# Kernel optimization log

Measured on AMD Instinct MI355X. Metric: run time of the kernel, lower is better.

## Reference

```python
import jax, jax.numpy as jnp
import numpy as np

DIM = 384
HEADS = 12
WS = 7            # per-side window size (sqrt of 49)
TOK = WS * WS     # tokens per window = 49


def _relative_position_index():
    coords = np.stack(np.meshgrid(np.arange(WS), np.arange(WS), indexing='ij'))  # [2,ws,ws]
    flat = coords.reshape(2, -1)                                                  # [2,49]
    rel = flat[:, :, None] - flat[:, None, :]                                     # [2,49,49]
    rel = rel.transpose(1, 2, 0)
    rel[:, :, 0] += WS - 1
    rel[:, :, 1] += WS - 1
    rel[:, :, 0] *= 2 * WS - 1
    return rel.sum(-1).astype(np.int32)                                           # [49,49]


def setup_inputs() -> dict:
    key = jax.random.key(0)
    ks = jax.random.split(key, 6)
    B, N, C = 32, 3136, DIM
    x = jax.random.normal(ks[0], (B, N, C), dtype=jnp.float32)
    qkv_w = jax.random.normal(ks[1], (C, 3 * C), dtype=jnp.float32) * 0.02
    qkv_b = jnp.zeros((3 * C,), dtype=jnp.float32)
    proj_w = jax.random.normal(ks[2], (C, C), dtype=jnp.float32) * 0.02
    proj_b = jnp.zeros((C,), dtype=jnp.float32)
    n_bias = (2 * WS - 1) * (2 * WS - 1)  # 169
    rel_bias_table = jax.random.normal(ks[3], (n_bias, HEADS), dtype=jnp.float32) * 0.02
    rel_index = jnp.asarray(_relative_position_index())
    return {"x": x, "qkv_w": qkv_w, "qkv_b": qkv_b, "proj_w": proj_w,
            "proj_b": proj_b, "rel_bias_table": rel_bias_table, "rel_index": rel_index}


def reference(x, qkv_w, qkv_b, proj_w, proj_b, rel_bias_table, rel_index):
    B, N, C = x.shape
    H, d = HEADS, C // HEADS
    L = N // TOK                      # number of windows per batch element
    scale = d ** (-0.5)

    qkv = x @ qkv_w + qkv_b                              # [B,N,3C]
    qkv = qkv.reshape(B * L, TOK, 3, H, d)               # non-shuffle layout: (L ws1 ws2)
    q = jnp.transpose(qkv[:, :, 0], (0, 2, 1, 3)) * scale  # [BL,H,49,d]
    k = jnp.transpose(qkv[:, :, 1], (0, 2, 1, 3))
    v = jnp.transpose(qkv[:, :, 2], (0, 2, 1, 3))

    attn = jnp.einsum('whqd,whkd->whqk', q, k)           # [BL,H,49,49]
    bias = rel_bias_table[rel_index.reshape(-1)].reshape(TOK, TOK, H)
    bias = jnp.transpose(bias, (2, 0, 1))                # [H,49,49]
    attn = jax.nn.softmax(attn + bias[None], axis=-1)

    out = jnp.einsum('whqk,whkd->whqd', attn, v)         # [BL,H,49,d]
    out = jnp.transpose(out, (0, 2, 1, 3)).reshape(B, N, C)
    return out @ proj_w + proj_b
```

## Files before the change

### kernel.cpp

```cpp
#include <hip/hip_runtime.h>
#include <stdint.h>

#define TOK 49
#define NTOK 100352
#define K3 1152
#define C_DIM 384
#define NHEAD 12

typedef _Float16 half8 __attribute__((ext_vector_type(8)));
typedef float f32x4 __attribute__((ext_vector_type(4)));

__device__ __forceinline__ ushort f2h_bits(float f) {
  _Float16 h = (_Float16)f;
  return __builtin_bit_cast(ushort, h);
}

__device__ __forceinline__ void gload_lds16(const void* gp, void* lp) {
  __builtin_amdgcn_global_load_lds(
      (const __attribute__((address_space(1))) void*)gp,
      (__attribute__((address_space(3))) void*)lp, 16, 0, 0);
}

__global__ __launch_bounds__(256) void cvt_f32_f16(const float* __restrict__ in,
                                                   _Float16* __restrict__ out, int n4) {
  int i = blockIdx.x * 256 + threadIdx.x;
  if (i >= n4) return;
  float4 v = *((const float4*)in + i);
  ushort4 o;
  o.x = f2h_bits(v.x); o.y = f2h_bits(v.y); o.z = f2h_bits(v.z); o.w = f2h_bits(v.w);
  *((ushort4*)out + i) = o;
}

__global__ __launch_bounds__(256) void transpose_to_f16(const float* __restrict__ in,
                                                        _Float16* __restrict__ out,
                                                        int R, int Cc) {
  int idx = blockIdx.x * 256 + threadIdx.x;
  if (idx >= R * Cc) return;
  int n = idx / R, k = idx - n * R;
  out[idx] = (_Float16)in[(size_t)k * Cc + n];
}

__global__ __launch_bounds__(256) void bias_expand(const float* __restrict__ table,
                                                   const int* __restrict__ relidx,
                                                   float* __restrict__ out) {
  int idx = blockIdx.x * 256 + threadIdx.x;
  if (idx >= NHEAD * TOK * TOK) return;
  int h = idx / (TOK * TOK);
  int qk = idx - h * (TOK * TOK);
  out[idx] = table[relidx[qk] * NHEAD + h];
}

template <int OUT_F32>
__global__ __launch_bounds__(256) void gemm_f16(const _Float16* __restrict__ A,
                                                const _Float16* __restrict__ Bt,
                                                const float* __restrict__ bias,
                                                void* __restrict__ Cout,
                                                int N, int K, int Ntiles) {
  __shared__ _Float16 As[128 * 32];
  __shared__ _Float16 Bs[128 * 32];
  int bid = blockIdx.x;
  int bm = bid / Ntiles, bn = bid - bm * Ntiles;
  int tid = threadIdx.x;
  int lane = tid & 63, wave = tid >> 6;
  int wm = wave >> 1, wn = wave & 1;

  int srow = tid >> 2;
  int scol = (tid & 3) * 8;
  const _Float16* gA = A + (size_t)(bm * 128 + srow) * K + scol;
  const _Float16* gB = Bt + (size_t)(bn * 128 + srow) * K + scol;
  char* ldsA = (char*)As + wave * 1024;
  char* ldsB = (char*)Bs + wave * 1024;

  f32x4 acc[4][4];
#pragma unroll
  for (int m = 0; m < 4; m++)
#pragma unroll
    for (int n = 0; n < 4; n++) acc[m][n] = (f32x4){0.f, 0.f, 0.f, 0.f};

  int fr = lane & 15;
  int fk = (lane >> 4) * 8;

  for (int k0 = 0; k0 < K; k0 += 32) {
    __syncthreads();
    gload_lds16(gA + k0, ldsA);
    gload_lds16(gA + (size_t)64 * K + k0, ldsA + 4096);
    gload_lds16(gB + k0, ldsB);
    gload_lds16(gB + (size_t)64 * K + k0, ldsB + 4096);
    __syncthreads();
    half8 af[4], bf[4];
#pragma unroll
    for (int m = 0; m < 4; m++)
      af[m] = *(const half8*)(As + (wm * 64 + m * 16 + fr) * 32 + fk);
#pragma unroll
    for (int n = 0; n < 4; n++)
      bf[n] = *(const half8*)(Bs + (wn * 64 + n * 16 + fr) * 32 + fk);
#pragma unroll
    for (int m = 0; m < 4; m++)
#pragma unroll
      for (int n = 0; n < 4; n++)
        acc[m][n] = __builtin_amdgcn_mfma_f32_16x16x32_f16(af[m], bf[n], acc[m][n], 0, 0, 0);
  }

  int rowbase = bm * 128 + wm * 64;
  int colbase = bn * 128 + wn * 64;
#pragma unroll
  for (int n = 0; n < 4; n++) {
    int col = colbase + n * 16 + fr;
    float bb = bias[col];
#pragma unroll
    for (int m = 0; m < 4; m++) {
      int row0 = rowbase + m * 16 + (lane >> 4) * 4;
#pragma unroll
      for (int r = 0; r < 4; r++) {
        float v = acc[m][n][r] + bb;
        if (OUT_F32)
          ((float*)Cout)[(size_t)(row0 + r) * N + col] = v;
        else
          ((ushort*)Cout)[(size_t)(row0 + r) * N + col] = f2h_bits(v);
      }
    }
  }
}

__global__ __launch_bounds__(256) void win_attn(const _Float16* __restrict__ qkv,
                                                const float* __restrict__ biasf,
                                                _Float16* __restrict__ aout) {
  __shared__ _Float16 P[4][64 * 72];
  int lane = threadIdx.x & 63, wave = threadIdx.x >> 6;
  int id = blockIdx.x * 4 + wave;
  int win = id / NHEAD;
  int h = id - win * NHEAD;
  const _Float16* base = qkv + (size_t)win * TOK * K3 + h * 32;
  int fr = lane & 15, fg = lane >> 4;

  half8 qf[4], kf[4];
#pragma unroll
  for (int i = 0; i < 4; i++) {
    int q = i * 16 + fr;
    qf[i] = (half8){0, 0, 0, 0, 0, 0, 0, 0};
    kf[i] = (half8){0, 0, 0, 0, 0, 0, 0, 0};
    if (q < TOK) {
      qf[i] = *(const half8*)(base + (size_t)q * K3 + fg * 8);
      kf[i] = *(const half8*)(base + (size_t)q * K3 + 384 + fg * 8);
    }
  }

  f32x4 s[4][4];
#pragma unroll
  for (int i = 0; i < 4; i++)
#pragma unroll
    for (int j = 0; j < 4; j++) s[i][j] = (f32x4){0.f, 0.f, 0.f, 0.f};
#pragma unroll
  for (int i = 0; i < 4; i++)
#pragma unroll
    for (int j = 0; j < 4; j++)
      s[i][j] = __builtin_amdgcn_mfma_f32_16x16x32_f16(qf[i], kf[j], s[i][j], 0, 0, 0);

  const float scale = 0.17677669529663687f;
  const float* bh = biasf + h * (TOK * TOK);
#pragma unroll
  for (int i = 0; i < 4; i++) {
#pragma unroll
    for (int r = 0; r < 4; r++) {
      int q = i * 16 + fg * 4 + r;
      float vals[4];
      float rowm = -1e30f;
#pragma unroll
      for (int j = 0; j < 4; j++) {
        int kk = j * 16 + fr;
        float v = -1e30f;
        if (q < TOK && kk < TOK) v = s[i][j][r] * scale + bh[q * TOK + kk];
        vals[j] = v;
        rowm = fmaxf(rowm, v);
      }
#pragma unroll
      for (int md = 1; md < 16; md <<= 1) rowm = fmaxf(rowm, __shfl_xor(rowm, md, 64));
      float rs = 0.f;
#pragma unroll
      for (int j = 0; j < 4; j++) { vals[j] = __expf(vals[j] - rowm); rs += vals[j]; }
#pragma unroll
      for (int md = 1; md < 16; md <<= 1) rs += __shfl_xor(rs, md, 64);
      float iv = 1.0f / rs;
#pragma unroll
      for (int j = 0; j < 4; j++)
        P[wave][q * 72 + j * 16 + fr] = (_Float16)(vals[j] * iv);
    }
  }

  half8 vf[2][2];
#pragma unroll
  for (int n = 0; n < 2; n++)
#pragma unroll
    for (int kx = 0; kx < 2; kx++) {
#pragma unroll
      for (int e = 0; e < 8; e++) {
        int kk = kx * 32 + fg * 8 + e;
        _Float16 vv = (_Float16)0.f;
        if (kk < TOK) vv = base[(size_t)kk * K3 + 768 + n * 16 + fr];
        vf[n][kx][e] = vv;
      }
    }

  f32x4 o[4][2];
#pragma unroll
  for (int i = 0; i < 4; i++)
#pragma unroll
    for (int n = 0; n < 2; n++) o[i][n] = (f32x4){0.f, 0.f, 0.f, 0.f};
#pragma unroll
  for (int i = 0; i < 4; i++) {
    half8 pf0 = *(const half8*)(&P[wave][(i * 16 + fr) * 72 + fg * 8]);
    half8 pf1 = *(const half8*)(&P[wave][(i * 16 + fr) * 72 + 32 + fg * 8]);
#pragma unroll
    for (int n = 0; n < 2; n++) {
      o[i][n] = __builtin_amdgcn_mfma_f32_16x16x32_f16(pf0, vf[n][0], o[i][n], 0, 0, 0);
      o[i][n] = __builtin_amdgcn_mfma_f32_16x16x32_f16(pf1, vf[n][1], o[i][n], 0, 0, 0);
    }
  }

  _Float16* obase = aout + (size_t)win * TOK * C_DIM + h * 32;
#pragma unroll
  for (int i = 0; i < 4; i++)
#pragma unroll
    for (int n = 0; n < 2; n++)
#pragma unroll
      for (int r = 0; r < 4; r++) {
        int q = i * 16 + fg * 4 + r;
        if (q < TOK) obase[(size_t)q * C_DIM + n * 16 + fr] = (_Float16)o[i][n][r];
      }
}

extern "C" void kernel_launch(void* const* d_in, const int* in_sizes, int n_in,
                              void* d_out, int out_size, void* d_ws, size_t ws_size,
                              hipStream_t stream) {
  const float* x = (const float*)d_in[0];
  const float* qkv_w = (const float*)d_in[1];
  const float* qkv_b = (const float*)d_in[2];
  const float* proj_w = (const float*)d_in[3];
  const float* proj_b = (const float*)d_in[4];
  const float* rel_table = (const float*)d_in[5];
  const int* rel_index = (const int*)d_in[6];

  char* ws = (char*)d_ws;
  _Float16* ws_x    = (_Float16*)(ws + 0);
  _Float16* ws_qkv  = (_Float16*)(ws + 77070336);
  _Float16* ws_attn = (_Float16*)(ws + 308281344);
  _Float16* ws_wT   = (_Float16*)(ws + 385351680);
  _Float16* ws_pT   = (_Float16*)(ws + 386236416);
  float*    ws_bias = (float*)(ws + 386531328);

  cvt_f32_f16<<<37632, 256, 0, stream>>>(x, ws_x, 9633792);
  transpose_to_f16<<<1728, 256, 0, stream>>>(qkv_w, ws_wT, 384, 1152);
  transpose_to_f16<<<576, 256, 0, stream>>>(proj_w, ws_pT, 384, 384);
  bias_expand<<<113, 256, 0, stream>>>(rel_table, rel_index, ws_bias);

  gemm_f16<0><<<7056, 256, 0, stream>>>(ws_x, ws_wT, qkv_b, ws_qkv, 1152, 384, 9);
  win_attn<<<6144, 256, 0, stream>>>(ws_qkv, ws_bias, ws_attn);
  gemm_f16<1><<<2352, 256, 0, stream>>>(ws_attn, ws_pT, proj_b, (void*)d_out, 384, 384, 3);
}
```

Baseline: 607.7 us.

## Double-buffer GEMM LDS tiles and hoist V loads in window attention

The GEMM kernel now keeps two LDS buffers for the A and B tiles and issues the global-to-LDS loads for the next K step before computing on the current one. This replaces the two barriers per iteration with a single waitcnt+barrier, aiming to overlap memory latency with MFMA work. The attention kernel also issues its scattered V gathers at the start, so their latency overlaps the QK^T and softmax phase. The cost is doubled LDS per GEMM block, which may lower occupancy, and more live registers in the attention kernel.

New measurement: 605.0 us. Within noise of the previous version (-0.4%).

```diff
diff --git a/kernel.cpp b/kernel.cpp
--- a/kernel.cpp
+++ b/kernel.cpp
@@ -56,8 +56,8 @@
                                                 const float* __restrict__ bias,
                                                 void* __restrict__ Cout,
                                                 int N, int K, int Ntiles) {
-  __shared__ _Float16 As[128 * 32];
-  __shared__ _Float16 Bs[128 * 32];
+  __shared__ _Float16 As[2][128 * 32];
+  __shared__ _Float16 Bs[2][128 * 32];
   int bid = blockIdx.x;
   int bm = bid / Ntiles, bn = bid - bm * Ntiles;
   int tid = threadIdx.x;
@@ -68,8 +68,6 @@
   int scol = (tid & 3) * 8;
   const _Float16* gA = A + (size_t)(bm * 128 + srow) * K + scol;
   const _Float16* gB = Bt + (size_t)(bn * 128 + srow) * K + scol;
-  char* ldsA = (char*)As + wave * 1024;
-  char* ldsB = (char*)Bs + wave * 1024;
 
   f32x4 acc[4][4];
 #pragma unroll
@@ -79,26 +77,40 @@
 
   int fr = lane & 15;
   int fk = (lane >> 4) * 8;
-
-  for (int k0 = 0; k0 < K; k0 += 32) {
-    __syncthreads();
-    gload_lds16(gA + k0, ldsA);
-    gload_lds16(gA + (size_t)64 * K + k0, ldsA + 4096);
-    gload_lds16(gB + k0, ldsB);
-    gload_lds16(gB + (size_t)64 * K + k0, ldsB + 4096);
-    __syncthreads();
+  int nk = K >> 5;
+
+  auto STAGE = [&](int buf, int k0) {
+    char* la = (char*)As[buf] + wave * 1024;
+    char* lb = (char*)Bs[buf] + wave * 1024;
+    gload_lds16(gA + k0, la);
+    gload_lds16(gA + (size_t)64 * K + k0, la + 4096);
+    gload_lds16(gB + k0, lb);
+    gload_lds16(gB + (size_t)64 * K + k0, lb + 4096);
+  };
+
+  STAGE(0, 0);
+  asm volatile("s_waitcnt vmcnt(0)" ::: "memory");
+  __builtin_amdgcn_s_barrier();
+
+  for (int t = 0; t < nk; t++) {
+    int cur = t & 1;
+    if (t + 1 < nk) STAGE(cur ^ 1, (t + 1) * 32);
     half8 af[4], bf[4];
 #pragma unroll
     for (int m = 0; m < 4; m++)
-      af[m] = *(const half8*)(As + (wm * 64 + m * 16 + fr) * 32 + fk);
+      af[m] = *(const half8*)(As[cur] + (wm * 64 + m * 16 + fr) * 32 + fk);
 #pragma unroll
     for (int n = 0; n < 4; n++)
-      bf[n] = *(const half8*)(Bs + (wn * 64 + n * 16 + fr) * 32 + fk);
+      bf[n] = *(const half8*)(Bs[cur] + (wn * 64 + n * 16 + fr) * 32 + fk);
 #pragma unroll
     for (int m = 0; m < 4; m++)
 #pragma unroll
       for (int n = 0; n < 4; n++)
         acc[m][n] = __builtin_amdgcn_mfma_f32_16x16x32_f16(af[m], bf[n], acc[m][n], 0, 0, 0);
+    if (t + 1 < nk) {
+      asm volatile("s_waitcnt vmcnt(0)" ::: "memory");
+      __builtin_amdgcn_s_barrier();
+    }
   }
 
   int rowbase = bm * 128 + wm * 64;
@@ -133,6 +145,20 @@
   const _Float16* base = qkv + (size_t)win * TOK * K3 + h * 32;
   int fr = lane & 15, fg = lane >> 4;
 
+  half8 vf[2][2];
+#pragma unroll
+  for (int n = 0; n < 2; n++)
+#pragma unroll
+    for (int kx = 0; kx < 2; kx++) {
+#pragma unroll
+      for (int e = 0; e < 8; e++) {
+        int kk = kx * 32 + fg * 8 + e;
+        _Float16 vv = (_Float16)0.f;
+        if (kk < TOK) vv = base[(size_t)kk * K3 + 768 + n * 16 + fr];
+        vf[n][kx][e] = vv;
+      }
+    }
+
   half8 qf[4], kf[4];
 #pragma unroll
   for (int i = 0; i < 4; i++) {
@@ -186,20 +212,6 @@
         P[wave][q * 72 + j * 16 + fr] = (_Float16)(vals[j] * iv);
     }
   }
-
-  half8 vf[2][2];
-#pragma unroll
-  for (int n = 0; n < 2; n++)
-#pragma unroll
-    for (int kx = 0; kx < 2; kx++) {
-#pragma unroll
-      for (int e = 0; e < 8; e++) {
-        int kk = kx * 32 + fg * 8 + e;
-        _Float16 vv = (_Float16)0.f;
-        if (kk < TOK) vv = base[(size_t)kk * K3 + 768 + n * 16 + fr];
-        vf[n][kx][e] = vv;
-      }
-    }
 
   f32x4 o[4][2];
 #pragma unroll
```
